# Performance work log

Hardware: AMD Instinct MI355X
Metric: run time of the kernel (lower is better)

Reference implementation:

```python
import jax, jax.numpy as jnp
import numpy as np

LAMBDA_TEMP = 20.0
GAMMA = 20.0
MARGIN = 0.05
EPS = 1e-8

B, K, M, D = 128, 256, 8, 128


def _unit(x, axis=-1):
    return x / jnp.linalg.norm(x, axis=axis, keepdims=True)


def setup_inputs() -> dict:
    key = jax.random.key(0)
    k1, k2, k3 = jax.random.split(key, 3)
    v_proj = _unit(jax.random.normal(k1, (B, K, D), dtype=jnp.float32))
    prototypes = _unit(jax.random.normal(k2, (K, M, D), dtype=jnp.float32))
    concept_labels = jax.random.randint(k3, (B, K), 0, 2, dtype=jnp.int64)
    return {"v_proj": v_proj, "concept_labels": concept_labels, "prototypes": prototypes}


def reference(v_proj, concept_labels, prototypes):
    # all-pairs prototype similarities: query vector (b,k) vs prototypes of concept c
    # sims: (B, K, C, M)
    sims = jnp.einsum('bkd,cmd->bkcm', v_proj, prototypes)
    # Eq.6: soft assignment over the M prototypes of each concept
    q = jax.nn.softmax(GAMMA * sims, axis=-1)
    # Eq.7-8: weighted similarity sim_c(v)  -> (B, K, C)
    sim = jnp.sum(q * sims, axis=-1)
    # positive similarity: concept k queried against its own prototypes, plus margin
    sim_pos = jnp.einsum('bkk->bk', sim) + MARGIN  # (B, K)
    # Eq.9: -log( exp(lam*sim_pos) / (sum_c exp(lam*sim_c) + eps) )
    denom = jnp.sum(jnp.exp(LAMBDA_TEMP * sim), axis=-1) + EPS  # (B, K)
    loss_bk = jnp.log(denom) - LAMBDA_TEMP * sim_pos  # (B, K)
    mask = (concept_labels == 1).astype(loss_bk.dtype)
    num_pos = jnp.sum(mask)
    total = jnp.sum(loss_bk * mask)
    return jnp.where(num_pos > 0, total / num_pos, total)
```

## Files before the change

kernel.cpp:

```cpp
#include <hip/hip_runtime.h>

#define LT     20.0f
#define C2EXP  28.853900817779268f
#define CHUNKS 16
#define NBLK   512

typedef _Float16 half8 __attribute__((ext_vector_type(8)));
typedef float    f32x4 __attribute__((ext_vector_type(4)));

#if __has_builtin(__builtin_amdgcn_exp2f)
#define EXP2F(x) __builtin_amdgcn_exp2f(x)
#else
#define EXP2F(x) __expf(0.69314718055994531f * (x))
#endif

__device__ __forceinline__ float swz16(float x) {
    return __int_as_float(__builtin_amdgcn_ds_swizzle(__float_as_int(x), 0x401F));
}

__global__ __launch_bounds__(256)
void mpcl_prep(const float* __restrict__ P, _Float16* __restrict__ Pw,
               int* __restrict__ ws)
{
    int id = blockIdx.x * 256 + threadIdx.x;
    if (id == 0) ws[0] = 0;
    int ch    = id >> 11;
    int colq  = (id >> 9) & 3;
    int cfrag = (id >> 6) & 7;
    int lane  = id & 63;
    int n = lane & 15, q = lane >> 4;
    int c = cfrag & 3, h = cfrag >> 2;
    int col  = colq * 32 + ((n >> 2) << 3) + (n & 3) + (h << 2);
    int gcol = (ch << 7) + col;
    const float* src = P + ((size_t)gcol << 7) + c * 32 + q * 8;
    float4 a = *(const float4*)src;
    float4 b = *(const float4*)(src + 4);
    half8 hv;
    hv[0] = (_Float16)a.x; hv[1] = (_Float16)a.y;
    hv[2] = (_Float16)a.z; hv[3] = (_Float16)a.w;
    hv[4] = (_Float16)b.x; hv[5] = (_Float16)b.y;
    hv[6] = (_Float16)b.z; hv[7] = (_Float16)b.w;
    *(half8*)(Pw + (size_t)id * 8) = hv;
}

__global__ __launch_bounds__(512, 4)
void mpcl_main(const float* __restrict__ V,
               const int*   __restrict__ labels,
               const _Float16* __restrict__ Pw,
               int* __restrict__ ws,
               float* __restrict__ out)
{
    __shared__ float sh_denom[64];
    __shared__ float sh_simpos[64];
    __shared__ float sh_fin[16];
    __shared__ int   sh_last;

    int*   gcnt = ws;
    float* part = (float*)((char*)ws + 256);

    const int tid  = threadIdx.x;
    const int lane = tid & 63;
    const int w    = tid >> 6;
    const int colq = w & 3;
    const int rg   = w >> 2;
    const int n    = lane & 15;
    const int q    = lane >> 4;
    const int rowbase = blockIdx.x * 64;

    if (tid < 64) { sh_denom[tid] = 0.0f; sh_simpos[tid] = 0.0f; }

    int lab = 0;
    if (tid < 64) lab = labels[rowbase + tid];

    half8 vh[2][4];
#pragma unroll
    for (int rf = 0; rf < 2; ++rf) {
        const float* vr = V + ((size_t)(rowbase + rg * 32 + rf * 16 + n) << 7) + q * 8;
#pragma unroll
        for (int c = 0; c < 4; ++c) {
            float4 x0 = *(const float4*)(vr + c * 32);
            float4 x1 = *(const float4*)(vr + c * 32 + 4);
            vh[rf][c][0] = (_Float16)x0.x; vh[rf][c][1] = (_Float16)x0.y;
            vh[rf][c][2] = (_Float16)x0.z; vh[rf][c][3] = (_Float16)x0.w;
            vh[rf][c][4] = (_Float16)x1.x; vh[rf][c][5] = (_Float16)x1.y;
            vh[rf][c][6] = (_Float16)x1.z; vh[rf][c][7] = (_Float16)x1.w;
        }
    }
    __syncthreads();

    const half8* pw = (const half8*)Pw + (size_t)colq * 512 + lane;

    const int rowk0 = (rowbase + rg * 32 + n) & 255;
    const int rowk1 = (rowbase + rg * 32 + 16 + n) & 255;

    float dn0 = 0.f, dn1 = 0.f;

    half8 bufA[8], bufB[8];
#pragma unroll
    for (int f = 0; f < 8; ++f) bufA[f] = pw[f * 64];

#define COMPUTE(BUF, CABASE) do {                                               \
    f32x4 acc1[2] = {{0.f,0.f,0.f,0.f},{0.f,0.f,0.f,0.f}};                      \
    f32x4 acc2[2] = {{0.f,0.f,0.f,0.f},{0.f,0.f,0.f,0.f}};                      \
    _Pragma("unroll")                                                           \
    for (int c = 0; c < 4; ++c) {                                               \
        acc1[0] = __builtin_amdgcn_mfma_f32_16x16x32_f16(BUF[c],   vh[0][c], acc1[0], 0, 0, 0); \
        acc1[1] = __builtin_amdgcn_mfma_f32_16x16x32_f16(BUF[c],   vh[1][c], acc1[1], 0, 0, 0); \
        acc2[0] = __builtin_amdgcn_mfma_f32_16x16x32_f16(BUF[4+c], vh[0][c], acc2[0], 0, 0, 0); \
        acc2[1] = __builtin_amdgcn_mfma_f32_16x16x32_f16(BUF[4+c], vh[1][c], acc2[1], 0, 0, 0); \
    }                                                                           \
    _Pragma("unroll")                                                           \
    for (int rf = 0; rf < 2; ++rf) {                                            \
        float x0 = acc1[rf][0], x1 = acc1[rf][1], x2 = acc1[rf][2], x3 = acc1[rf][3]; \
        float x4 = acc2[rf][0], x5 = acc2[rf][1], x6 = acc2[rf][2], x7 = acc2[rf][3]; \
        float e0 = EXP2F(C2EXP * x0), e1 = EXP2F(C2EXP * x1);                   \
        float e2 = EXP2F(C2EXP * x2), e3 = EXP2F(C2EXP * x3);                   \
        float e4 = EXP2F(C2EXP * x4), e5 = EXP2F(C2EXP * x5);                   \
        float e6 = EXP2F(C2EXP * x6), e7 = EXP2F(C2EXP * x7);                   \
        float es = ((e0 + e1) + (e2 + e3)) + ((e4 + e5) + (e6 + e7));           \
        float ss = fmaf(e0, x0, fmaf(e1, x1, fmaf(e2, x2, e3 * x3)))            \
                 + fmaf(e4, x4, fmaf(e5, x5, fmaf(e6, x6, e7 * x7)));           \
        float simc = __fdividef(ss, es);                                        \
        if (rf) dn1 += EXP2F(C2EXP * simc); else dn0 += EXP2F(C2EXP * simc);    \
        if ((CABASE) == (rf ? rowk1 : rowk0))                                   \
            sh_simpos[rg * 32 + rf * 16 + n] = simc;         \
    }                                                                           \
} while (0)

    int cA = colq * 4 + q;
#pragma unroll 1
    for (int ch = 0; ch < CHUNKS; ch += 2) {
#pragma unroll
        for (int f = 0; f < 8; ++f) bufB[f] = pw[(ch + 1) * 2048 + f * 64];

        COMPUTE(bufA, cA);

        if (ch + 2 < CHUNKS) {
#pragma unroll
            for (int f = 0; f < 8; ++f) bufA[f] = pw[(ch + 2) * 2048 + f * 64];
        }

        COMPUTE(bufB, cA + 16);
        cA += 32;
    }

#pragma unroll
    for (int rf = 0; rf < 2; ++rf) {
        float t = rf ? dn1 : dn0;
        t += swz16(t);
        t += __shfl_xor(t, 32);
        if (lane < 16)
            atomicAdd(&sh_denom[rg * 32 + rf * 16 + n], t);
    }
    __syncthreads();

    float s = 0.f, cc = 0.f;
    if (tid < 64) {
        float lp = logf(sh_denom[tid] + 1e-8f) - LT * (sh_simpos[tid] + 0.05f);
        float mk = (lab == 1) ? 1.0f : 0.0f;
        s = lp * mk;
        cc = mk;
    }
#pragma unroll
    for (int off = 32; off >= 1; off >>= 1) {
        s  += __shfl_down(s, off);
        cc += __shfl_down(cc, off);
    }

    if (tid == 0) {
        __hip_atomic_store(&part[2 * blockIdx.x],     s,  __ATOMIC_RELAXED, __HIP_MEMORY_SCOPE_AGENT);
        __hip_atomic_store(&part[2 * blockIdx.x + 1], cc, __ATOMIC_RELAXED, __HIP_MEMORY_SCOPE_AGENT);
        __threadfence();
        int g = __hip_atomic_fetch_add(gcnt, 1, __ATOMIC_ACQ_REL, __HIP_MEMORY_SCOPE_AGENT);
        sh_last = (g == NBLK - 1);
    }
    __syncthreads();
    if (sh_last) {
        float ts = 0.f, tc = 0.f;
        for (int i = tid; i < NBLK; i += 512) {
            ts += __hip_atomic_load(&part[2 * i],     __ATOMIC_RELAXED, __HIP_MEMORY_SCOPE_AGENT);
            tc += __hip_atomic_load(&part[2 * i + 1], __ATOMIC_RELAXED, __HIP_MEMORY_SCOPE_AGENT);
        }
#pragma unroll
        for (int off = 32; off >= 1; off >>= 1) {
            ts += __shfl_down(ts, off);
            tc += __shfl_down(tc, off);
        }
        if (lane == 0) { sh_fin[w] = ts; sh_fin[8 + w] = tc; }
        __syncthreads();
        if (tid == 0) {
            ts = 0.f; tc = 0.f;
#pragma unroll
            for (int i = 0; i < 8; ++i) { ts += sh_fin[i]; tc += sh_fin[8 + i]; }
            out[0] = (tc > 0.0f) ? (ts / tc) : ts;
        }
    }
}

extern "C" void kernel_launch(void* const* d_in, const int* in_sizes, int n_in,
                              void* d_out, int out_size, void* d_ws, size_t ws_size,
                              hipStream_t stream)
{
    const float* V      = (const float*)d_in[0];
    const int*   labels = (const int*)d_in[1];
    const float* P      = (const float*)d_in[2];
    float* out = (float*)d_out;
    int*   ws  = (int*)d_ws;
    _Float16* Pw = (_Float16*)((char*)d_ws + 16384);

    mpcl_prep<<<128, 256, 0, stream>>>(P, Pw, ws);
    mpcl_main<<<NBLK, 512, 0, stream>>>(V, labels, Pw, ws, out);
}
```

Before: 111.7 us.

## Prescale prototypes by exp constant, replicate weights, pin occupancy and schedule barriers

Folds the lambda/log2 scaling into the fp16 prototype conversion, so the main loop computes exp2 directly on MFMA outputs and the final loss is rescaled with ln2. The prep kernel writes 8 copies of the packed prototypes and each block reads the copy chosen by blockIdx&7, meant to spread L2/cache-channel contention. It also swaps launch_bounds for an explicit waves-per-eu of 3 and adds sched_barriers around the prefetch loads. Prescaling by about 28.85 before fp16 rounding shifts where precision is lost, and the prep kernel now does 8x the writes.

After: 112.5 us. Within noise of the previous version (+0.8%).

```diff
diff --git a/kernel.cpp b/kernel.cpp
--- a/kernel.cpp
+++ b/kernel.cpp
@@ -1,9 +1,11 @@
 #include <hip/hip_runtime.h>
 
-#define LT     20.0f
-#define C2EXP  28.853900817779268f
-#define CHUNKS 16
-#define NBLK   512
+#define LT      20.0f
+#define LN2     0.69314718055994531f
+#define C2EXP   28.853900817779268f
+#define CHUNKS  16
+#define NBLK    512
+#define PW_COPY 262144
 
 typedef _Float16 half8 __attribute__((ext_vector_type(8)));
 typedef float    f32x4 __attribute__((ext_vector_type(4)));
@@ -22,8 +24,9 @@
 void mpcl_prep(const float* __restrict__ P, _Float16* __restrict__ Pw,
                int* __restrict__ ws)
 {
-    int id = blockIdx.x * 256 + threadIdx.x;
-    if (id == 0) ws[0] = 0;
+    if (blockIdx.x == 0 && threadIdx.x == 0) ws[0] = 0;
+    int copy = blockIdx.x & 7;
+    int id   = (blockIdx.x >> 3) * 256 + threadIdx.x;
     int ch    = id >> 11;
     int colq  = (id >> 9) & 3;
     int cfrag = (id >> 6) & 7;
@@ -36,14 +39,15 @@
     float4 a = *(const float4*)src;
     float4 b = *(const float4*)(src + 4);
     half8 hv;
-    hv[0] = (_Float16)a.x; hv[1] = (_Float16)a.y;
-    hv[2] = (_Float16)a.z; hv[3] = (_Float16)a.w;
-    hv[4] = (_Float16)b.x; hv[5] = (_Float16)b.y;
-    hv[6] = (_Float16)b.z; hv[7] = (_Float16)b.w;
-    *(half8*)(Pw + (size_t)id * 8) = hv;
-}
-
-__global__ __launch_bounds__(512, 4)
+    hv[0] = (_Float16)(C2EXP * a.x); hv[1] = (_Float16)(C2EXP * a.y);
+    hv[2] = (_Float16)(C2EXP * a.z); hv[3] = (_Float16)(C2EXP * a.w);
+    hv[4] = (_Float16)(C2EXP * b.x); hv[5] = (_Float16)(C2EXP * b.y);
+    hv[6] = (_Float16)(C2EXP * b.z); hv[7] = (_Float16)(C2EXP * b.w);
+    *(half8*)(Pw + (size_t)copy * PW_COPY + (size_t)id * 8) = hv;
+}
+
+__global__ __attribute__((amdgpu_flat_work_group_size(512, 512),
+                          amdgpu_waves_per_eu(3, 3)))
 void mpcl_main(const float* __restrict__ V,
                const int*   __restrict__ labels,
                const _Float16* __restrict__ Pw,
@@ -88,7 +92,8 @@
     }
     __syncthreads();
 
-    const half8* pw = (const half8*)Pw + (size_t)colq * 512 + lane;
+    const half8* pw = (const half8*)(Pw + (size_t)(blockIdx.x & 7) * PW_COPY)
+                    + (size_t)colq * 512 + lane;
 
     const int rowk0 = (rowbase + rg * 32 + n) & 255;
     const int rowk1 = (rowbase + rg * 32 + 16 + n) & 255;
@@ -113,17 +118,15 @@
     for (int rf = 0; rf < 2; ++rf) {                                            \
         float x0 = acc1[rf][0], x1 = acc1[rf][1], x2 = acc1[rf][2], x3 = acc1[rf][3]; \
         float x4 = acc2[rf][0], x5 = acc2[rf][1], x6 = acc2[rf][2], x7 = acc2[rf][3]; \
-        float e0 = EXP2F(C2EXP * x0), e1 = EXP2F(C2EXP * x1);                   \
-        float e2 = EXP2F(C2EXP * x2), e3 = EXP2F(C2EXP * x3);                   \
-        float e4 = EXP2F(C2EXP * x4), e5 = EXP2F(C2EXP * x5);                   \
-        float e6 = EXP2F(C2EXP * x6), e7 = EXP2F(C2EXP * x7);                   \
+        float e0 = EXP2F(x0), e1 = EXP2F(x1), e2 = EXP2F(x2), e3 = EXP2F(x3);   \
+        float e4 = EXP2F(x4), e5 = EXP2F(x5), e6 = EXP2F(x6), e7 = EXP2F(x7);   \
         float es = ((e0 + e1) + (e2 + e3)) + ((e4 + e5) + (e6 + e7));           \
         float ss = fmaf(e0, x0, fmaf(e1, x1, fmaf(e2, x2, e3 * x3)))            \
                  + fmaf(e4, x4, fmaf(e5, x5, fmaf(e6, x6, e7 * x7)));           \
-        float simc = __fdividef(ss, es);                                        \
-        if (rf) dn1 += EXP2F(C2EXP * simc); else dn0 += EXP2F(C2EXP * simc);    \
+        float simY = __fdividef(ss, es);                   \
+        if (rf) dn1 += EXP2F(simY); else dn0 += EXP2F(simY);                    \
         if ((CABASE) == (rf ? rowk1 : rowk0))                                   \
-            sh_simpos[rg * 32 + rf * 16 + n] = simc;         \
+            sh_simpos[rg * 32 + rf * 16 + n] = simY;         \
     }                                                                           \
 } while (0)
 
@@ -132,6 +135,7 @@
     for (int ch = 0; ch < CHUNKS; ch += 2) {
 #pragma unroll
         for (int f = 0; f < 8; ++f) bufB[f] = pw[(ch + 1) * 2048 + f * 64];
+        __builtin_amdgcn_sched_barrier(0);
 
         COMPUTE(bufA, cA);
 
@@ -139,6 +143,7 @@
 #pragma unroll
             for (int f = 0; f < 8; ++f) bufA[f] = pw[(ch + 2) * 2048 + f * 64];
         }
+        __builtin_amdgcn_sched_barrier(0);
 
         COMPUTE(bufB, cA + 16);
         cA += 32;
@@ -156,7 +161,7 @@
 
     float s = 0.f, cc = 0.f;
     if (tid < 64) {
-        float lp = logf(sh_denom[tid] + 1e-8f) - LT * (sh_simpos[tid] + 0.05f);
+        float lp = logf(sh_denom[tid] + 1e-8f) - LN2 * sh_simpos[tid] - 1.0f;
         float mk = (lab == 1) ? 1.0f : 0.0f;
         s = lp * mk;
         cc = mk;
@@ -208,6 +213,6 @@
     int*   ws  = (int*)d_ws;
     _Float16* Pw = (_Float16*)((char*)d_ws + 16384);
 
-    mpcl_prep<<<128, 256, 0, stream>>>(P, Pw, ws);
+    mpcl_prep<<<1024, 256, 0, stream>>>(P, Pw, ws);
     mpcl_main<<<NBLK, 512, 0, stream>>>(V, labels, Pw, ws, out);
 }
```
